# Kernel optimization log

Measured on AMD Instinct MI355X. Metric: run time of the kernel, lower is better.

Reference implementation:

```python
import jax, jax.numpy as jnp
import numpy as np

MARGIN_POS = 1.0
MARGIN_NEG = 0.2
LAMBDA_D = 250.0

B, D, H, W = 2, 128, 64, 64


def setup_inputs() -> dict:
    key = jax.random.key(0)
    k0, k1, k2 = jax.random.split(key, 3)
    descriptors_0 = jax.random.normal(k0, (B, D, H, W), dtype=jnp.float32)
    descriptors_1 = jax.random.normal(k1, (B, D, H, W), dtype=jnp.float32)
    similarity_mask = jax.random.randint(k2, (B, H, W, H, W), 0, 2).astype(jnp.bool_)
    return {
        "descriptors_0": descriptors_0,
        "descriptors_1": descriptors_1,
        "similarity_mask": similarity_mask,
    }


def reference(descriptors_0, descriptors_1, similarity_mask):
    # [B,D,H,W] x [B,D,H,W] -> [B,H,W,H,W] dense pairwise descriptor dot products
    dotprod = jnp.einsum('bdij,bdkl->bijkl', descriptors_0, descriptors_1)
    zero = jnp.zeros((), dtype=dotprod.dtype)
    pos_loss = jnp.maximum(zero, MARGIN_POS - dotprod) * LAMBDA_D
    neg_loss = jnp.maximum(zero, dotprod - MARGIN_NEG)
    return jnp.where(similarity_mask, pos_loss, neg_loss).mean()
```

## Files before the change

### kernel.cpp

```cpp
#include <hip/hip_runtime.h>
#include <hip/hip_bf16.h>
#include <stdint.h>

#define BN 2
#define DN 128
#define MN 4096
#define TOTAL_INV (1.0f / 33554432.0f)

typedef __attribute__((ext_vector_type(8))) short short8;
typedef __attribute__((ext_vector_type(4))) float f32x4;

__device__ static inline unsigned short f2bf(float x) {
  unsigned int u = __float_as_uint(x);
  u += 0x7fffu + ((u >> 16) & 1u);
  return (unsigned short)(u >> 16);
}

__device__ static inline void async16(const void* g, void* l) {
  __builtin_amdgcn_global_load_lds(
      (const __attribute__((address_space(1))) void*)g,
      (__attribute__((address_space(3))) void*)l, 16, 0, 0);
}

__global__ __launch_bounds__(256) void transpose_cvt(
    const float* __restrict__ s0, const float* __restrict__ s1,
    unsigned short* __restrict__ o0, unsigned short* __restrict__ o1) {
  __shared__ float tile[64][65];
  const int tx = threadIdx.x & 63;
  const int ty = threadIdx.x >> 6;
  const int m0 = blockIdx.x * 64;
  const int d0 = blockIdx.y * 64;
  const int b  = blockIdx.z & 1;
  const float* src = (blockIdx.z >> 1) ? s1 : s0;
  unsigned short* dst = (blockIdx.z >> 1) ? o1 : o0;
  src += (size_t)b * DN * MN;
  dst += (size_t)b * MN * DN;
#pragma unroll
  for (int i = 0; i < 16; ++i) {
    int dr = i * 4 + ty;
    tile[dr][tx] = src[(size_t)(d0 + dr) * MN + m0 + tx];
  }
  __syncthreads();
#pragma unroll
  for (int i = 0; i < 16; ++i) {
    int mr = i * 4 + ty;
    dst[(size_t)(m0 + mr) * DN + d0 + tx] = f2bf(tile[tx][mr]);
  }
}

__global__ __launch_bounds__(256) void gemm_loss(
    const unsigned short* __restrict__ A, const unsigned short* __restrict__ Bm,
    const void* __restrict__ maskp, float* __restrict__ out) {
  __shared__ __align__(16) unsigned short As[128 * 32];
  __shared__ __align__(16) unsigned short Bs[128 * 32];
  __shared__ float red[4];
  __shared__ int mask_is_u8;

  const int tid  = threadIdx.x;
  const int lane = tid & 63;
  const int wave = tid >> 6;
  const int wm = wave >> 1, wn = wave & 1;
  const int quad = lane >> 4;
  const int l16  = lane & 15;
  const int bn = blockIdx.x, bm = blockIdx.y, bz = blockIdx.z;

  if (tid == 0) mask_is_u8 = 0;
  __syncthreads();
  if (((const unsigned int*)maskp)[tid] & 0xFFFFFF00u) mask_is_u8 = 1;

  const unsigned short* Ab = A  + (size_t)bz * MN * DN + (size_t)(bm * 128) * DN;
  const unsigned short* Bb = Bm + (size_t)bz * MN * DN + (size_t)(bn * 128) * DN;

  f32x4 acc[4][4];
#pragma unroll
  for (int i = 0; i < 4; ++i)
#pragma unroll
    for (int j = 0; j < 4; ++j) acc[i][j] = (f32x4){0.f, 0.f, 0.f, 0.f};

#pragma unroll
  for (int kt = 0; kt < 4; ++kt) {
    const int k0 = kt * 32;
#pragma unroll
    for (int p = 0; p < 2; ++p) {
      int c = tid + p * 256;
      int row = c >> 2;
      int cq  = c & 3;
      async16(Ab + (size_t)row * DN + k0 + cq * 8, As + c * 8);
      async16(Bb + (size_t)row * DN + k0 + cq * 8, Bs + c * 8);
    }
    __syncthreads();

    short8 af[4], bf[4];
#pragma unroll
    for (int mi = 0; mi < 4; ++mi)
      af[mi] = *(const short8*)(As + (wm * 64 + mi * 16 + l16) * 32 + quad * 8);
#pragma unroll
    for (int ni = 0; ni < 4; ++ni)
      bf[ni] = *(const short8*)(Bs + (wn * 64 + ni * 16 + l16) * 32 + quad * 8);
#pragma unroll
    for (int mi = 0; mi < 4; ++mi)
#pragma unroll
      for (int ni = 0; ni < 4; ++ni)
        acc[mi][ni] = __builtin_amdgcn_mfma_f32_16x16x32_bf16(
            af[mi], bf[ni], acc[mi][ni], 0, 0, 0);
    __syncthreads();
  }

  const size_t mbase =
      ((size_t)bz * MN + (size_t)(bm * 128 + wm * 64)) * MN + (size_t)(bn * 128 + wn * 64);
  const int* mi32 = (const int*)maskp;
  const unsigned char* mu8 = (const unsigned char*)maskp;
  const int u8 = mask_is_u8;
  float lsum = 0.0f;
#pragma unroll
  for (int mi = 0; mi < 4; ++mi) {
#pragma unroll
    for (int ni = 0; ni < 4; ++ni) {
      f32x4 v = acc[mi][ni];
#pragma unroll
      for (int r = 0; r < 4; ++r) {
        int m = mi * 16 + quad * 4 + r;
        int n = ni * 16 + l16;
        size_t idx = mbase + (size_t)m * MN + n;
        int msk = u8 ? (int)mu8[idx] : mi32[idx];
        float dot = v[r];
        float pos = fmaxf(0.0f, 1.0f - dot) * 250.0f;
        float neg = fmaxf(0.0f, dot - 0.2f);
        lsum += msk ? pos : neg;
      }
    }
  }
#pragma unroll
  for (int off = 32; off > 0; off >>= 1) lsum += __shfl_xor(lsum, off);
  if (lane == 0) red[wave] = lsum;
  __syncthreads();
  if (tid == 0) {
    float t = (red[0] + red[1] + red[2] + red[3]) * TOTAL_INV;
    atomicAdd(out, t);
  }
}

extern "C" void kernel_launch(void* const* d_in, const int* in_sizes, int n_in,
                              void* d_out, int out_size, void* d_ws, size_t ws_size,
                              hipStream_t stream) {
  const float* d0 = (const float*)d_in[0];
  const float* d1 = (const float*)d_in[1];
  const void* mask = d_in[2];
  float* out = (float*)d_out;

  unsigned short* Aw = (unsigned short*)d_ws;
  unsigned short* Bw = Aw + (size_t)BN * MN * DN;

  hipMemsetAsync(d_out, 0, sizeof(float), stream);

  dim3 g1(MN / 64, DN / 64, BN * 2), b1(256);
  transpose_cvt<<<g1, b1, 0, stream>>>(d0, d1, Aw, Bw);

  dim3 g2(MN / 128, MN / 128, BN), b2(256);
  gemm_loss<<<g2, b2, 0, stream>>>(Aw, Bw, mask, out);
}
```

Measured before the change: 209.2 us.

## Stage mask tile into LDS with async loads before GEMM loop

The mask tile for each 128x128 output block is now fetched into a 64KB shared buffer with 16-byte async global-to-LDS loads, issued before the K loop. This replaces the scattered per-element byte or int loads in the epilogue, and the fetch can overlap with the A/B loads and MFMA work. It also folds the output zeroing into the transpose kernel, drops the final block reduction in favour of per-wave atomics, and skips the last barrier. The large static LDS allocation reduces how many blocks can be resident per CU.

```diff
diff --git a/kernel.cpp b/kernel.cpp
--- a/kernel.cpp
+++ b/kernel.cpp
@@ -24,7 +24,10 @@
 
 __global__ __launch_bounds__(256) void transpose_cvt(
     const float* __restrict__ s0, const float* __restrict__ s1,
-    unsigned short* __restrict__ o0, unsigned short* __restrict__ o1) {
+    unsigned short* __restrict__ o0, unsigned short* __restrict__ o1,
+    float* __restrict__ outp) {
+  if (threadIdx.x == 0 && blockIdx.x == 0 && blockIdx.y == 0 && blockIdx.z == 0)
+    *outp = 0.0f;
   __shared__ float tile[64][65];
   const int tx = threadIdx.x & 63;
   const int ty = threadIdx.x >> 6;
@@ -53,8 +56,7 @@
     const void* __restrict__ maskp, float* __restrict__ out) {
   __shared__ __align__(16) unsigned short As[128 * 32];
   __shared__ __align__(16) unsigned short Bs[128 * 32];
-  __shared__ float red[4];
-  __shared__ int mask_is_u8;
+  __shared__ __align__(16) unsigned char Ms[128 * 128 * 4];
 
   const int tid  = threadIdx.x;
   const int lane = tid & 63;
@@ -64,9 +66,27 @@
   const int l16  = lane & 15;
   const int bn = blockIdx.x, bm = blockIdx.y, bz = blockIdx.z;
 
-  if (tid == 0) mask_is_u8 = 0;
-  __syncthreads();
-  if (((const unsigned int*)maskp)[tid] & 0xFFFFFF00u) mask_is_u8 = 1;
+  unsigned sw = ((const unsigned int*)maskp)[lane];
+  const bool mask_u8 = (__ballot((sw & 0xFFFFFF00u) != 0u) != 0ull);
+
+  const size_t mrow0 = ((size_t)bz * MN + (size_t)(bm * 128)) * MN + (size_t)(bn * 128);
+  if (mask_u8) {
+    const unsigned char* mg = (const unsigned char*)maskp + mrow0;
+#pragma unroll
+    for (int p = 0; p < 4; ++p) {
+      int c = tid + p * 256;
+      int row = c >> 3, col = (c & 7) << 4;
+      async16(mg + (size_t)row * MN + col, Ms + (size_t)c * 16);
+    }
+  } else {
+    const unsigned char* mg = (const unsigned char*)maskp + mrow0 * 4;
+#pragma unroll
+    for (int p = 0; p < 16; ++p) {
+      int c = tid + p * 256;
+      int row = c >> 5, col = (c & 31) << 4;
+      async16(mg + (size_t)row * (MN * 4) + col, Ms + (size_t)c * 16);
+    }
+  }
 
   const unsigned short* Ab = A  + (size_t)bz * MN * DN + (size_t)(bm * 128) * DN;
   const unsigned short* Bb = Bm + (size_t)bz * MN * DN + (size_t)(bn * 128) * DN;
@@ -85,8 +105,8 @@
       int c = tid + p * 256;
       int row = c >> 2;
       int cq  = c & 3;
-      async16(Ab + (size_t)row * DN + k0 + cq * 8, As + c * 8);
-      async16(Bb + (size_t)row * DN + k0 + cq * 8, Bs + c * 8);
+      async16(Ab + (size_t)row * DN + k0 + cq * 8, As + (size_t)c * 8);
+      async16(Bb + (size_t)row * DN + k0 + cq * 8, Bs + (size_t)c * 8);
     }
     __syncthreads();
 
@@ -103,14 +123,13 @@
       for (int ni = 0; ni < 4; ++ni)
         acc[mi][ni] = __builtin_amdgcn_mfma_f32_16x16x32_bf16(
             af[mi], bf[ni], acc[mi][ni], 0, 0, 0);
-    __syncthreads();
+    if (kt != 3) __syncthreads();
   }
 
-  const size_t mbase =
-      ((size_t)bz * MN + (size_t)(bm * 128 + wm * 64)) * MN + (size_t)(bn * 128 + wn * 64);
-  const int* mi32 = (const int*)maskp;
-  const unsigned char* mu8 = (const unsigned char*)maskp;
-  const int u8 = mask_is_u8;
+  const unsigned char* Mu8 = Ms;
+  const unsigned int*  Mi  = (const unsigned int*)Ms;
+  const int mrow = wm * 64 + quad * 4;
+  const int ncol = wn * 64 + l16;
   float lsum = 0.0f;
 #pragma unroll
   for (int mi = 0; mi < 4; ++mi) {
@@ -119,10 +138,8 @@
       f32x4 v = acc[mi][ni];
 #pragma unroll
       for (int r = 0; r < 4; ++r) {
-        int m = mi * 16 + quad * 4 + r;
-        int n = ni * 16 + l16;
-        size_t idx = mbase + (size_t)m * MN + n;
-        int msk = u8 ? (int)mu8[idx] : mi32[idx];
+        int idx = (mrow + mi * 16 + r) * 128 + (ncol + ni * 16);
+        int msk = mask_u8 ? (int)Mu8[idx] : (int)Mi[idx];
         float dot = v[r];
         float pos = fmaxf(0.0f, 1.0f - dot) * 250.0f;
         float neg = fmaxf(0.0f, dot - 0.2f);
@@ -132,12 +149,7 @@
   }
 #pragma unroll
   for (int off = 32; off > 0; off >>= 1) lsum += __shfl_xor(lsum, off);
-  if (lane == 0) red[wave] = lsum;
-  __syncthreads();
-  if (tid == 0) {
-    float t = (red[0] + red[1] + red[2] + red[3]) * TOTAL_INV;
-    atomicAdd(out, t);
-  }
+  if (lane == 0) atomicAdd(out, lsum * TOTAL_INV);
 }
 
 extern "C" void kernel_launch(void* const* d_in, const int* in_sizes, int n_in,
@@ -151,10 +163,8 @@
   unsigned short* Aw = (unsigned short*)d_ws;
   unsigned short* Bw = Aw + (size_t)BN * MN * DN;
 
-  hipMemsetAsync(d_out, 0, sizeof(float), stream);
-
   dim3 g1(MN / 64, DN / 64, BN * 2), b1(256);
-  transpose_cvt<<<g1, b1, 0, stream>>>(d0, d1, Aw, Bw);
+  transpose_cvt<<<g1, b1, 0, stream>>>(d0, d1, Aw, Bw, out);
 
   dim3 g2(MN / 128, MN / 128, BN), b2(256);
   gemm_loss<<<g2, b2, 0, stream>>>(Aw, Bw, mask, out);
```

Measured after the change: 279.5 us. 33.6% more time.

## Load MFMA operands directly from global memory, drop LDS staging and barriers

Applied to the files above, without the earlier changes.

The GEMM kernel stops staging A/B tiles through LDS with async loads and block barriers. Each wave now loads its bf16 fragments straight from global memory into registers, with the k-loop left unrolled only once. The same change folds the output zeroing into the transpose kernel instead of a separate memset, detects the mask format per wave with a ballot, and does one atomic per wave instead of a block reduction. It trades LDS reuse between waves for more global and L2 traffic, and adds an occupancy hint of three blocks per CU; the kernel is likely dominated by the mask read anyway.

```diff
diff --git a/kernel.cpp b/kernel.cpp
--- a/kernel.cpp
+++ b/kernel.cpp
@@ -16,15 +16,12 @@
   return (unsigned short)(u >> 16);
 }
 
-__device__ static inline void async16(const void* g, void* l) {
-  __builtin_amdgcn_global_load_lds(
-      (const __attribute__((address_space(1))) void*)g,
-      (__attribute__((address_space(3))) void*)l, 16, 0, 0);
-}
-
 __global__ __launch_bounds__(256) void transpose_cvt(
     const float* __restrict__ s0, const float* __restrict__ s1,
-    unsigned short* __restrict__ o0, unsigned short* __restrict__ o1) {
+    unsigned short* __restrict__ o0, unsigned short* __restrict__ o1,
+    float* __restrict__ outp) {
+  if (threadIdx.x == 0 && blockIdx.x == 0 && blockIdx.y == 0 && blockIdx.z == 0)
+    *outp = 0.0f;
   __shared__ float tile[64][65];
   const int tx = threadIdx.x & 63;
   const int ty = threadIdx.x >> 6;
@@ -48,28 +45,24 @@
   }
 }
 
-__global__ __launch_bounds__(256) void gemm_loss(
+__global__ __launch_bounds__(256, 3) void gemm_loss(
     const unsigned short* __restrict__ A, const unsigned short* __restrict__ Bm,
     const void* __restrict__ maskp, float* __restrict__ out) {
-  __shared__ __align__(16) unsigned short As[128 * 32];
-  __shared__ __align__(16) unsigned short Bs[128 * 32];
-  __shared__ float red[4];
-  __shared__ int mask_is_u8;
-
   const int tid  = threadIdx.x;
   const int lane = tid & 63;
   const int wave = tid >> 6;
   const int wm = wave >> 1, wn = wave & 1;
   const int quad = lane >> 4;
   const int l16  = lane & 15;
-  const int bn = blockIdx.x, bm = blockIdx.y, bz = blockIdx.z;
+  const int bz = blockIdx.z;
+  const int gm = blockIdx.y * 128 + wm * 64;
+  const int gn = blockIdx.x * 128 + wn * 64;
 
-  if (tid == 0) mask_is_u8 = 0;
-  __syncthreads();
-  if (((const unsigned int*)maskp)[tid] & 0xFFFFFF00u) mask_is_u8 = 1;
+  unsigned sw = ((const unsigned int*)maskp)[lane];
+  const bool mask_u8 = (__ballot((sw & 0xFFFFFF00u) != 0u) != 0ull);
 
-  const unsigned short* Ab = A  + (size_t)bz * MN * DN + (size_t)(bm * 128) * DN;
-  const unsigned short* Bb = Bm + (size_t)bz * MN * DN + (size_t)(bn * 128) * DN;
+  const unsigned short* Ab = A  + (size_t)bz * MN * DN + (size_t)gm * DN;
+  const unsigned short* Bb = Bm + (size_t)bz * MN * DN + (size_t)gn * DN;
 
   f32x4 acc[4][4];
 #pragma unroll
@@ -77,40 +70,27 @@
 #pragma unroll
     for (int j = 0; j < 4; ++j) acc[i][j] = (f32x4){0.f, 0.f, 0.f, 0.f};
 
-#pragma unroll
+#pragma unroll 1
   for (int kt = 0; kt < 4; ++kt) {
-    const int k0 = kt * 32;
-#pragma unroll
-    for (int p = 0; p < 2; ++p) {
-      int c = tid + p * 256;
-      int row = c >> 2;
-      int cq  = c & 3;
-      async16(Ab + (size_t)row * DN + k0 + cq * 8, As + c * 8);
-      async16(Bb + (size_t)row * DN + k0 + cq * 8, Bs + c * 8);
-    }
-    __syncthreads();
-
+    const int k0 = kt * 32 + quad * 8;
     short8 af[4], bf[4];
 #pragma unroll
     for (int mi = 0; mi < 4; ++mi)
-      af[mi] = *(const short8*)(As + (wm * 64 + mi * 16 + l16) * 32 + quad * 8);
+      af[mi] = *(const short8*)(Ab + (size_t)(mi * 16 + l16) * DN + k0);
 #pragma unroll
     for (int ni = 0; ni < 4; ++ni)
-      bf[ni] = *(const short8*)(Bs + (wn * 64 + ni * 16 + l16) * 32 + quad * 8);
+      bf[ni] = *(const short8*)(Bb + (size_t)(ni * 16 + l16) * DN + k0);
 #pragma unroll
     for (int mi = 0; mi < 4; ++mi)
 #pragma unroll
       for (int ni = 0; ni < 4; ++ni)
         acc[mi][ni] = __builtin_amdgcn_mfma_f32_16x16x32_bf16(
             af[mi], bf[ni], acc[mi][ni], 0, 0, 0);
-    __syncthreads();
   }
 
-  const size_t mbase =
-      ((size_t)bz * MN + (size_t)(bm * 128 + wm * 64)) * MN + (size_t)(bn * 128 + wn * 64);
+  const size_t mbase = ((size_t)bz * MN + (size_t)gm) * MN + (size_t)gn;
   const int* mi32 = (const int*)maskp;
   const unsigned char* mu8 = (const unsigned char*)maskp;
-  const int u8 = mask_is_u8;
   float lsum = 0.0f;
 #pragma unroll
   for (int mi = 0; mi < 4; ++mi) {
@@ -122,7 +102,7 @@
         int m = mi * 16 + quad * 4 + r;
         int n = ni * 16 + l16;
         size_t idx = mbase + (size_t)m * MN + n;
-        int msk = u8 ? (int)mu8[idx] : mi32[idx];
+        int msk = mask_u8 ? (int)mu8[idx] : mi32[idx];
         float dot = v[r];
         float pos = fmaxf(0.0f, 1.0f - dot) * 250.0f;
         float neg = fmaxf(0.0f, dot - 0.2f);
@@ -132,12 +112,7 @@
   }
 #pragma unroll
   for (int off = 32; off > 0; off >>= 1) lsum += __shfl_xor(lsum, off);
-  if (lane == 0) red[wave] = lsum;
-  __syncthreads();
-  if (tid == 0) {
-    float t = (red[0] + red[1] + red[2] + red[3]) * TOTAL_INV;
-    atomicAdd(out, t);
-  }
+  if (lane == 0) atomicAdd(out, lsum * TOTAL_INV);
 }
 
 extern "C" void kernel_launch(void* const* d_in, const int* in_sizes, int n_in,
@@ -151,10 +126,8 @@
   unsigned short* Aw = (unsigned short*)d_ws;
   unsigned short* Bw = Aw + (size_t)BN * MN * DN;
 
-  hipMemsetAsync(d_out, 0, sizeof(float), stream);
-
   dim3 g1(MN / 64, DN / 64, BN * 2), b1(256);
-  transpose_cvt<<<g1, b1, 0, stream>>>(d0, d1, Aw, Bw);
+  transpose_cvt<<<g1, b1, 0, stream>>>(d0, d1, Aw, Bw, out);
 
   dim3 g2(MN / 128, MN / 128, BN), b2(256);
   gemm_loss<<<g2, b2, 0, stream>>>(Aw, Bw, mask, out);
```

Result: slower. 295.1 us (+41.0%).
